# Kernel optimization log

Measured on AMD Instinct MI355X. Metric: run time of the kernel, lower is better.

## Reference

```python
import jax, jax.numpy as jnp
import numpy as np

N_NODES = 100000
N_EDGES = 1200000
NODE_IN = 64
EDGE_IN = 32
HIDDEN = 64


def _glorot(key, shape):
    fan_in, fan_out = shape[0], shape[1]
    s = jnp.sqrt(2.0 / (fan_in + fan_out))
    return jax.random.normal(key, shape, dtype=jnp.float32) * s


def setup_inputs() -> dict:
    key = jax.random.key(0)
    ks = jax.random.split(key, 16)
    inp = {
        "x": jax.random.normal(ks[0], (N_NODES, NODE_IN), dtype=jnp.float32),
        "edge_index": jax.random.randint(ks[1], (2, N_EDGES), 0, N_NODES, dtype=jnp.int64),
        "edge_attr": jax.random.normal(ks[2], (N_EDGES, EDGE_IN), dtype=jnp.float32),
        # SAGE layer 0 (in=NODE_IN -> HIDDEN): lin_l (neighbors, has bias), lin_r (root)
        "w_l0": _glorot(ks[3], (NODE_IN, HIDDEN)),
        "w_r0": _glorot(ks[4], (NODE_IN, HIDDEN)),
        "b0": jnp.zeros((HIDDEN,), jnp.float32),
        "ln_g0": jnp.ones((HIDDEN,), jnp.float32),
        "ln_b0": jnp.zeros((HIDDEN,), jnp.float32),
        # SAGE layer 1 (HIDDEN -> HIDDEN)
        "w_l1": _glorot(ks[5], (HIDDEN, HIDDEN)),
        "w_r1": _glorot(ks[6], (HIDDEN, HIDDEN)),
        "b1": jnp.zeros((HIDDEN,), jnp.float32),
        "ln_g1": jnp.ones((HIDDEN,), jnp.float32),
        "ln_b1": jnp.zeros((HIDDEN,), jnp.float32),
        # Edge classifier MLP: in_dim = 3*HIDDEN + EDGE_IN = 224
        "cw1": _glorot(ks[7], (3 * HIDDEN + EDGE_IN, HIDDEN)),
        "cb1": jnp.zeros((HIDDEN,), jnp.float32),
        "cw2": _glorot(ks[8], (HIDDEN, HIDDEN // 2)),
        "cb2": jnp.zeros((HIDDEN // 2,), jnp.float32),
        "cw3": _glorot(ks[9], (HIDDEN // 2, 1)),
        "cb3": jnp.zeros((1,), jnp.float32),
    }
    return inp


def _sage_conv(x, src, dst, w_l, w_r, b):
    # mean-aggregate source features at destination nodes (PyG SAGEConv, aggr='mean')
    n = x.shape[0]
    msg = x[src]  # [E, F] gather
    agg = jax.ops.segment_sum(msg, dst, num_segments=n)
    cnt = jax.ops.segment_sum(jnp.ones((src.shape[0], 1), x.dtype), dst, num_segments=n)
    mean = agg / jnp.maximum(cnt, 1.0)
    return mean @ w_l + x @ w_r + b


def _layer_norm(x, g, b, eps=1e-5):
    mu = jnp.mean(x, axis=-1, keepdims=True)
    var = jnp.var(x, axis=-1, keepdims=True)
    return (x - mu) * jax.lax.rsqrt(var + eps) * g + b


def reference(x, edge_index, edge_attr,
              w_l0, w_r0, b0, ln_g0, ln_b0,
              w_l1, w_r1, b1, ln_g1, ln_b1,
              cw1, cb1, cw2, cb2, cw3, cb3):
    src, dst = edge_index[0], edge_index[1]
    # Encoder (eval mode: dropout is identity)
    h = jax.nn.relu(_layer_norm(_sage_conv(x, src, dst, w_l0, w_r0, b0), ln_g0, ln_b0))
    z = jax.nn.relu(_layer_norm(_sage_conv(h, src, dst, w_l1, w_r1, b1), ln_g1, ln_b1))
    # Edge classifier: gather-concat-MLP
    z_src = z[src]
    z_dst = z[dst]
    edge_repr = jnp.concatenate([z_src, z_dst, z_src * z_dst, edge_attr], axis=-1)
    h1 = jax.nn.relu(edge_repr @ cw1 + cb1)
    h2 = jax.nn.relu(h1 @ cw2 + cb2)
    logits = (h2 @ cw3 + cb3).squeeze(-1)  # [E]
    return logits
```

## Files before the change

kernel.cpp:

```cpp
#include <hip/hip_runtime.h>
#include <hip/hip_bf16.h>

#define N_NODES 100000
#define N_EDGES 1200000

typedef __attribute__((ext_vector_type(8))) short bfrag;
typedef __attribute__((ext_vector_type(4))) float ffrag;

union FragU { uint4 v; uint32_t u[4]; bfrag f; };

__device__ __forceinline__ ushort bfbits(float a) {
  union { __hip_bfloat16 h; ushort u; } c; c.h = __float2bfloat16(a); return c.u;
}
__device__ __forceinline__ uint32_t pkbf(float a, float b) {
  union { __hip_bfloat162 h; uint32_t u; } c;
  c.h = __float22bfloat162_rn(float2{a, b}); return c.u;
}
__device__ __forceinline__ uint32_t mul2bf(uint32_t a, uint32_t b) {
  union { uint32_t u; __hip_bfloat162 h; } x, y, r;
  x.u = a; y.u = b; r.h = __hmul2(x.h, y.h); return r.u;
}
__device__ __forceinline__ float bflo(uint32_t u) { return __int_as_float(u << 16); }
__device__ __forceinline__ float bfhi(uint32_t u) { return __int_as_float(u & 0xffff0000u); }


__global__ void cvt_k(const float* __restrict__ x, ushort* __restrict__ xb, int n2) {
  int i = blockIdx.x * blockDim.x + threadIdx.x;
  if (i < n2) {
    float2 v = ((const float2*)x)[i];
    ((uint32_t*)xb)[i] = pkbf(v.x, v.y);
  }
}


__global__ void hist_k(const int* __restrict__ ei, int* __restrict__ deg, int E) {
  int e = blockIdx.x * blockDim.x + threadIdx.x;
  if (e < E) atomicAdd(&deg[ei[E + e]], 1);
}

__global__ __launch_bounds__(1024) void scan1_k(const int* __restrict__ deg,
                                                int* __restrict__ off,
                                                int* __restrict__ bsum, int n) {
  __shared__ int wpart[16];
  __shared__ int wpre[16];
  int tid = threadIdx.x, lane = tid & 63, wid = tid >> 6;
  int i = blockIdx.x * 1024 + tid;
  int v = (i < n) ? deg[i] : 0;
  int x = v;
  #pragma unroll
  for (int o = 1; o < 64; o <<= 1) {
    int y = __shfl_up(x, o);
    if (lane >= o) x += y;
  }
  if (lane == 63) wpart[wid] = x;
  __syncthreads();
  if (tid == 0) {
    int run = 0;
    #pragma unroll
    for (int w = 0; w < 16; w++) { int t = wpart[w]; wpre[w] = run; run += t; }
    bsum[blockIdx.x] = run;
  }
  __syncthreads();
  if (i < n) off[i] = x - v + wpre[wid];
}

__global__ void scan2_k(const int* __restrict__ bsum, int* __restrict__ bpre,
                        int* __restrict__ off, int nb, int n) {
  if (threadIdx.x == 0) {
    int run = 0;
    for (int b = 0; b < nb; b++) { int t = bsum[b]; bpre[b] = run; run += t; }
    off[n] = run;
  }
}

__global__ __launch_bounds__(1024) void scan3_k(int* __restrict__ off, int* __restrict__ pos,
                                                const int* __restrict__ bpre, int n) {
  int i = blockIdx.x * 1024 + threadIdx.x;
  if (i < n) {
    int o = off[i] + bpre[blockIdx.x];
    off[i] = o;
    pos[i] = o;
  }
}

__global__ void fill_k(const int* __restrict__ ei, int* __restrict__ pos,
                       int* __restrict__ csr, int E) {
  int e = blockIdx.x * blockDim.x + threadIdx.x;
  if (e < E) {
    int d = ei[E + e];
    int p = atomicAdd(&pos[d], 1);
    csr[p] = ei[e];
  }
}


__global__ __launch_bounds__(256) void agg_k(
    const ushort* __restrict__ Xb, const int* __restrict__ off, const int* __restrict__ csr,
    ushort* __restrict__ aggout, int n) {
  int lane = threadIdx.x & 63;
  int quad = lane >> 4, f8 = lane & 15;
  int wave = blockIdx.x * 4 + (threadIdx.x >> 6);
  int nw = gridDim.x * 4;
  int nquads = (n + 3) >> 2;
  const uint2* X2 = (const uint2*)Xb;
  for (int p = wave; p < nquads; p += nw) {
    int i = p * 4 + quad;
    int ic = i < n ? i : n - 1;
    int s0 = off[ic], s1 = off[ic + 1];
    float a0 = 0.f, a1 = 0.f, a2 = 0.f, a3 = 0.f;
    for (int j = s0; j < s1; j += 8) {
      int id[8]; uint2 us[8];
      #pragma unroll
      for (int u = 0; u < 8; u++) {
        int jj = j + u;
        id[u] = csr[jj < s1 ? jj : s1 - 1];
      }
      #pragma unroll
      for (int u = 0; u < 8; u++) us[u] = X2[(size_t)id[u] * 16 + f8];
      #pragma unroll
      for (int u = 0; u < 8; u++) {
        if (j + u < s1) {
          a0 += bflo(us[u].x); a1 += bfhi(us[u].x);
          a2 += bflo(us[u].y); a3 += bfhi(us[u].y);
        }
      }
    }
    if (i < n) {
      float rdeg = 1.f / fmaxf((float)(s1 - s0), 1.f);
      uint2 w;
      w.x = pkbf(a0 * rdeg, a1 * rdeg);
      w.y = pkbf(a2 * rdeg, a3 * rdeg);
      ((uint2*)aggout)[(size_t)i * 16 + f8] = w;
    }
  }
}


__global__ __launch_bounds__(256) void node_k(
    const ushort* __restrict__ agg, const ushort* __restrict__ selfb,
    const float* __restrict__ wl, const float* __restrict__ wr,
    const float* __restrict__ bias, const float* __restrict__ g, const float* __restrict__ lb,
    ushort* __restrict__ outb, int n) {
  __shared__ ushort wt[64 * 128];
  const int tid = threadIdx.x;
  for (int i = tid; i < 8192; i += 256) {
    int k = i >> 6, nn = i & 63;
    float v = (k < 64) ? wl[k * 64 + nn] : wr[(k - 64) * 64 + nn];
    wt[nn * 128 + (((k >> 3) ^ (nn & 7)) * 8) + (k & 7)] = bfbits(v);
  }
  __syncthreads();
  const int lane = tid & 63, wid = tid >> 6;
  const int ln = lane & 15, q = lane >> 4;
  float bias_n[4], g_n[4], lb_n[4];
  #pragma unroll
  for (int nt = 0; nt < 4; nt++) {
    bias_n[nt] = bias[nt * 16 + ln];
    g_n[nt] = g[nt * 16 + ln];
    lb_n[nt] = lb[nt * 16 + ln];
  }
  const int ntiles = (n + 15) >> 4;
  for (int t = blockIdx.x * 4 + wid; t < ntiles; t += gridDim.x * 4) {
    int node = t * 16 + ln;
    int nc = node < n ? node : n - 1;
    FragU afr[4];
    #pragma unroll
    for (int kk = 0; kk < 2; kk++) {
      afr[kk].v     = ((const uint4*)agg)[(size_t)nc * 8 + kk * 4 + q];
      afr[2 + kk].v = ((const uint4*)selfb)[(size_t)nc * 8 + kk * 4 + q];
    }
    ffrag acc[4];
    #pragma unroll
    for (int nt = 0; nt < 4; nt++) acc[nt] = ffrag{0.f, 0.f, 0.f, 0.f};
    #pragma unroll
    for (int kk = 0; kk < 4; kk++) {
      bfrag a = afr[kk].f;
      #pragma unroll
      for (int nt = 0; nt < 4; nt++) {
        int nn = nt * 16 + ln;
        int b = kk * 4 + q;
        const bfrag* bp = (const bfrag*)&wt[nn * 128 + ((b ^ (nn & 7)) * 8)];
        acc[nt] = __builtin_amdgcn_mfma_f32_16x16x32_bf16(a, *bp, acc[nt], 0, 0, 0);
      }
    }
    #pragma unroll
    for (int r = 0; r < 4; r++) {
      int m = t * 16 + q * 4 + r;
      float o[4];
      #pragma unroll
      for (int nt = 0; nt < 4; nt++) o[nt] = acc[nt][r] + bias_n[nt];
      float s = (o[0] + o[1]) + (o[2] + o[3]);
      #pragma unroll
      for (int mm = 1; mm < 16; mm <<= 1) s += __shfl_xor(s, mm);
      float mu = s * (1.f / 64.f);
      float v2 = 0.f;
      #pragma unroll
      for (int nt = 0; nt < 4; nt++) { float d2 = o[nt] - mu; v2 += d2 * d2; }
      #pragma unroll
      for (int mm = 1; mm < 16; mm <<= 1) v2 += __shfl_xor(v2, mm);
      float rs = rsqrtf(v2 * (1.f / 64.f) + 1e-5f);
      if (m < n) {
        #pragma unroll
        for (int nt = 0; nt < 4; nt++) {
          float y = fmaxf((o[nt] - mu) * rs * g_n[nt] + lb_n[nt], 0.f);
          outb[(size_t)m * 64 + nt * 16 + ln] = bfbits(y);
        }
      }
    }
  }
}


__global__ __launch_bounds__(256, 2) void edge_mfma_k(
    const int* __restrict__ ei, const float* __restrict__ ea,
    const ushort* __restrict__ zb,
    const float* __restrict__ cw1, const float* __restrict__ cb1,
    const float* __restrict__ cw2, const float* __restrict__ cb2,
    const float* __restrict__ cw3, const float* __restrict__ cb3,
    float* __restrict__ out, int E) {
  __shared__ ushort h1b[4][16 * 64];
  const int tid = threadIdx.x;
  const int lane = tid & 63, wid = tid >> 6;
  const int ln = lane & 15, q = lane >> 4;

  FragU w1f[7][4];
  #pragma unroll
  for (int kk = 0; kk < 7; kk++) {
    #pragma unroll
    for (int tt = 0; tt < 4; tt++) {
      #pragma unroll
      for (int p = 0; p < 4; p++) {
        int k = (kk * 4 + q) * 8 + p * 2;
        int n = tt * 16 + ln;
        w1f[kk][tt].u[p] = pkbf(cw1[k * 64 + n], cw1[(k + 1) * 64 + n]);
      }
    }
  }
  FragU w2f[2][2];
  #pragma unroll
  for (int t2 = 0; t2 < 2; t2++) {
    #pragma unroll
    for (int kk = 0; kk < 2; kk++) {
      #pragma unroll
      for (int p = 0; p < 4; p++) {
        int k = kk * 32 + q * 8 + p * 2;
        int n = t2 * 16 + ln;
        w2f[t2][kk].u[p] = pkbf(cw2[k * 32 + n], cw2[(k + 1) * 32 + n]);
      }
    }
  }

  float cb1v[4];
  #pragma unroll
  for (int t = 0; t < 4; t++) cb1v[t] = cb1[t * 16 + ln];
  float cb2a = cb2[ln], cb2b = cb2[16 + ln];
  float w3a = cw3[ln], w3b = cw3[16 + ln];
  float cb3v = cb3[0];

  ushort* hb = h1b[wid];
  const int ntiles = E >> 4;
  for (int t = blockIdx.x * 4 + wid; t < ntiles; t += gridDim.x * 4) {
    int e = t * 16 + ln;
    int s = ei[e], d = ei[E + e];

    FragU afr[7];
    #pragma unroll
    for (int kk = 0; kk < 2; kk++) {
      afr[kk].v     = ((const uint4*)zb)[(size_t)s * 8 + kk * 4 + q];
      afr[2 + kk].v = ((const uint4*)zb)[(size_t)d * 8 + kk * 4 + q];
    }
    {
      float4 lo = ((const float4*)ea)[(size_t)e * 8 + q * 2];
      float4 hi = ((const float4*)ea)[(size_t)e * 8 + q * 2 + 1];
      afr[6].u[0] = pkbf(lo.x, lo.y); afr[6].u[1] = pkbf(lo.z, lo.w);
      afr[6].u[2] = pkbf(hi.x, hi.y); afr[6].u[3] = pkbf(hi.z, hi.w);
    }
    #pragma unroll
    for (int kk = 0; kk < 2; kk++) {
      #pragma unroll
      for (int p = 0; p < 4; p++)
        afr[4 + kk].u[p] = mul2bf(afr[kk].u[p], afr[2 + kk].u[p]);
    }

    ffrag acc1[4];
    #pragma unroll
    for (int tt = 0; tt < 4; tt++) acc1[tt] = ffrag{0.f, 0.f, 0.f, 0.f};
    #pragma unroll
    for (int kk = 0; kk < 7; kk++) {
      bfrag a = afr[kk].f;
      #pragma unroll
      for (int tt = 0; tt < 4; tt++)
        acc1[tt] = __builtin_amdgcn_mfma_f32_16x16x32_bf16(a, w1f[kk][tt].f, acc1[tt], 0, 0, 0);
    }

    #pragma unroll
    for (int tt = 0; tt < 4; tt++) {
      #pragma unroll
      for (int r = 0; r < 4; r++) {
        int m = q * 4 + r;
        int col = tt * 16 + ln;
        float v = fmaxf(acc1[tt][r] + cb1v[tt], 0.f);
        hb[m * 64 + (((col >> 3) ^ (m & 7)) * 8) + (col & 7)] = bfbits(v);
      }
    }

    ffrag acc2[2];
    acc2[0] = ffrag{0.f, 0.f, 0.f, 0.f};
    acc2[1] = ffrag{0.f, 0.f, 0.f, 0.f};
    #pragma unroll
    for (int kk = 0; kk < 2; kk++) {
      int b = kk * 4 + q;
      const bfrag* ap = (const bfrag*)&hb[ln * 64 + ((b ^ (ln & 7)) * 8)];
      bfrag a2 = *ap;
      acc2[0] = __builtin_amdgcn_mfma_f32_16x16x32_bf16(a2, w2f[0][kk].f, acc2[0], 0, 0, 0);
      acc2[1] = __builtin_amdgcn_mfma_f32_16x16x32_bf16(a2, w2f[1][kk].f, acc2[1], 0, 0, 0);
    }

    float p0, p1, p2, p3;
    {
      p0 = fmaxf(acc2[0][0] + cb2a, 0.f) * w3a + fmaxf(acc2[1][0] + cb2b, 0.f) * w3b;
      p1 = fmaxf(acc2[0][1] + cb2a, 0.f) * w3a + fmaxf(acc2[1][1] + cb2b, 0.f) * w3b;
      p2 = fmaxf(acc2[0][2] + cb2a, 0.f) * w3a + fmaxf(acc2[1][2] + cb2b, 0.f) * w3b;
      p3 = fmaxf(acc2[0][3] + cb2a, 0.f) * w3a + fmaxf(acc2[1][3] + cb2b, 0.f) * w3b;
    }
    #pragma unroll
    for (int o = 1; o < 16; o <<= 1) {
      p0 += __shfl_xor(p0, o);
      p1 += __shfl_xor(p1, o);
      p2 += __shfl_xor(p2, o);
      p3 += __shfl_xor(p3, o);
    }
    float keep = (ln == 0) ? p0 : (ln == 1) ? p1 : (ln == 2) ? p2 : p3;
    if (ln < 4) out[t * 16 + q * 4 + ln] = keep + cb3v;
  }
}


extern "C" void kernel_launch(void* const* d_in, const int* in_sizes, int n_in,
                              void* d_out, int out_size, void* d_ws, size_t ws_size,
                              hipStream_t stream) {
  const float* x   = (const float*)d_in[0];
  const int*   ei  = (const int*)d_in[1];
  const float* ea  = (const float*)d_in[2];
  const float* wl0 = (const float*)d_in[3];
  const float* wr0 = (const float*)d_in[4];
  const float* b0  = (const float*)d_in[5];
  const float* g0  = (const float*)d_in[6];
  const float* lb0 = (const float*)d_in[7];
  const float* wl1 = (const float*)d_in[8];
  const float* wr1 = (const float*)d_in[9];
  const float* b1  = (const float*)d_in[10];
  const float* g1  = (const float*)d_in[11];
  const float* lb1 = (const float*)d_in[12];
  const float* cw1 = (const float*)d_in[13];
  const float* cb1 = (const float*)d_in[14];
  const float* cw2 = (const float*)d_in[15];
  const float* cb2 = (const float*)d_in[16];
  const float* cw3 = (const float*)d_in[17];
  const float* cb3 = (const float*)d_in[18];
  float* out = (float*)d_out;
  const int N = N_NODES, E = N_EDGES;
  const int NB = (N + 1023) / 1024;

  uintptr_t pp = (uintptr_t)d_ws;
  auto alloc = [&](size_t bytes) {
    uintptr_t r = (pp + 255) & ~(uintptr_t)255; pp = r + bytes; return (void*)r;
  };
  int* deg  = (int*)alloc((size_t)N * 4);
  int* off  = (int*)alloc((size_t)(N + 1) * 4);
  int* pos  = (int*)alloc((size_t)N * 4);
  int* csr  = (int*)alloc((size_t)E * 4);
  int* bsum = (int*)alloc((size_t)NB * 4);
  int* bpre = (int*)alloc((size_t)NB * 4);
  ushort* xb  = (ushort*)alloc((size_t)N * 64 * 2);
  ushort* agg = (ushort*)alloc((size_t)N * 64 * 2);
  ushort* hb  = (ushort*)alloc((size_t)N * 64 * 2);
  ushort* zb  = (ushort*)alloc((size_t)N * 64 * 2);

  hipMemsetAsync(deg, 0, (size_t)N * 4, stream);
  cvt_k<<<(N * 32 + 255) / 256, 256, 0, stream>>>(x, xb, N * 32);
  hist_k<<<(E + 255) / 256, 256, 0, stream>>>(ei, deg, E);
  scan1_k<<<NB, 1024, 0, stream>>>(deg, off, bsum, N);
  scan2_k<<<1, 64, 0, stream>>>(bsum, bpre, off, NB, N);
  scan3_k<<<NB, 1024, 0, stream>>>(off, pos, bpre, N);
  fill_k<<<(E + 255) / 256, 256, 0, stream>>>(ei, pos, csr, E);
  agg_k<<<2048, 256, 0, stream>>>(xb, off, csr, agg, N);
  node_k<<<512, 256, 0, stream>>>(agg, xb, wl0, wr0, b0, g0, lb0, hb, N);
  agg_k<<<2048, 256, 0, stream>>>(hb, off, csr, agg, N);
  node_k<<<512, 256, 0, stream>>>(agg, hb, wl1, wr1, b1, g1, lb1, zb, N);
  edge_mfma_k<<<512, 256, 0, stream>>>(ei, ea, zb, cw1, cb1, cw2, cb2, cw3, cb3, out, E);
}
```

Baseline: 561.2 us.

## Prefetch next edge tile, stage classifier weights in LDS, atomic-free CSR fill

The edge classifier now keeps the first-layer weights in swizzled LDS instead of 112 VGPRs per lane. This frees registers so the launch-bounds occupancy hint can be dropped and the grid doubled. It also software-pipelines the gather of the next tile's node embeddings and edge attributes behind the current tile's MFMA work. The CSR build records each edge's rank from the histogram atomic and fills without a second atomic pass, using nontemporal stores. Costs are extra LDS reads per MFMA, a per-block weight staging step, and an extra E-sized rank buffer.

```diff
diff --git a/kernel.cpp b/kernel.cpp
--- a/kernel.cpp
+++ b/kernel.cpp
@@ -33,9 +33,10 @@
 }
 
 
-__global__ void hist_k(const int* __restrict__ ei, int* __restrict__ deg, int E) {
+__global__ void hist_k(const int* __restrict__ ei, int* __restrict__ deg,
+                       int* __restrict__ rank, int E) {
   int e = blockIdx.x * blockDim.x + threadIdx.x;
-  if (e < E) atomicAdd(&deg[ei[E + e]], 1);
+  if (e < E) rank[e] = atomicAdd(&deg[ei[E + e]], 1);
 }
 
 __global__ __launch_bounds__(1024) void scan1_k(const int* __restrict__ deg,
@@ -73,23 +74,19 @@
   }
 }
 
-__global__ __launch_bounds__(1024) void scan3_k(int* __restrict__ off, int* __restrict__ pos,
+__global__ __launch_bounds__(1024) void scan3_k(int* __restrict__ off,
                                                 const int* __restrict__ bpre, int n) {
   int i = blockIdx.x * 1024 + threadIdx.x;
-  if (i < n) {
-    int o = off[i] + bpre[blockIdx.x];
-    off[i] = o;
-    pos[i] = o;
-  }
-}
-
-__global__ void fill_k(const int* __restrict__ ei, int* __restrict__ pos,
-                       int* __restrict__ csr, int E) {
+  if (i < n) off[i] += bpre[blockIdx.x];
+}
+
+__global__ void fill_k(const int* __restrict__ ei, const int* __restrict__ off,
+                       const int* __restrict__ rank, int* __restrict__ csr, int E) {
   int e = blockIdx.x * blockDim.x + threadIdx.x;
   if (e < E) {
     int d = ei[E + e];
-    int p = atomicAdd(&pos[d], 1);
-    csr[p] = ei[e];
+    int p = off[d] + rank[e];
+    __builtin_nontemporal_store(ei[e], &csr[p]);
   }
 }
 
@@ -210,44 +207,26 @@
 }
 
 
-__global__ __launch_bounds__(256, 2) void edge_mfma_k(
+__global__ __launch_bounds__(256) void edge_mfma_k(
     const int* __restrict__ ei, const float* __restrict__ ea,
     const ushort* __restrict__ zb,
     const float* __restrict__ cw1, const float* __restrict__ cb1,
     const float* __restrict__ cw2, const float* __restrict__ cb2,
     const float* __restrict__ cw3, const float* __restrict__ cb3,
     float* __restrict__ out, int E) {
+  __shared__ ushort wt1[64 * 256];
   __shared__ ushort h1b[4][16 * 64];
   const int tid = threadIdx.x;
+
+  for (int i = tid; i < 224 * 64; i += 256) {
+    int k = i >> 6, n = i & 63;
+    int blk = k >> 3;
+    wt1[n * 256 + ((blk ^ (n & 7)) * 8) + (k & 7)] = bfbits(cw1[i]);
+  }
+  __syncthreads();
+
   const int lane = tid & 63, wid = tid >> 6;
   const int ln = lane & 15, q = lane >> 4;
-
-  FragU w1f[7][4];
-  #pragma unroll
-  for (int kk = 0; kk < 7; kk++) {
-    #pragma unroll
-    for (int tt = 0; tt < 4; tt++) {
-      #pragma unroll
-      for (int p = 0; p < 4; p++) {
-        int k = (kk * 4 + q) * 8 + p * 2;
-        int n = tt * 16 + ln;
-        w1f[kk][tt].u[p] = pkbf(cw1[k * 64 + n], cw1[(k + 1) * 64 + n]);
-      }
-    }
-  }
-  FragU w2f[2][2];
-  #pragma unroll
-  for (int t2 = 0; t2 < 2; t2++) {
-    #pragma unroll
-    for (int kk = 0; kk < 2; kk++) {
-      #pragma unroll
-      for (int p = 0; p < 4; p++) {
-        int k = kk * 32 + q * 8 + p * 2;
-        int n = t2 * 16 + ln;
-        w2f[t2][kk].u[p] = pkbf(cw2[k * 32 + n], cw2[(k + 1) * 32 + n]);
-      }
-    }
-  }
 
   float cb1v[4];
   #pragma unroll
@@ -256,30 +235,61 @@
   float w3a = cw3[ln], w3b = cw3[16 + ln];
   float cb3v = cb3[0];
 
+  FragU w2f[2][2];
+  #pragma unroll
+  for (int t2 = 0; t2 < 2; t2++) {
+    #pragma unroll
+    for (int kk = 0; kk < 2; kk++) {
+      #pragma unroll
+      for (int p = 0; p < 4; p++) {
+        int k = kk * 32 + q * 8 + p * 2;
+        int n = t2 * 16 + ln;
+        w2f[t2][kk].u[p] = pkbf(cw2[k * 32 + n], cw2[(k + 1) * 32 + n]);
+      }
+    }
+  }
+
   ushort* hb = h1b[wid];
   const int ntiles = E >> 4;
-  for (int t = blockIdx.x * 4 + wid; t < ntiles; t += gridDim.x * 4) {
+  const int stride = gridDim.x * 4;
+  int t = blockIdx.x * 4 + wid;
+
+  FragU curz[4]; float4 ceal, ceah;
+  if (t < ntiles) {
     int e = t * 16 + ln;
     int s = ei[e], d = ei[E + e];
+    curz[0].v = ((const uint4*)zb)[(size_t)s * 8 + q];
+    curz[1].v = ((const uint4*)zb)[(size_t)s * 8 + 4 + q];
+    curz[2].v = ((const uint4*)zb)[(size_t)d * 8 + q];
+    curz[3].v = ((const uint4*)zb)[(size_t)d * 8 + 4 + q];
+    ceal = ((const float4*)ea)[(size_t)e * 8 + q * 2];
+    ceah = ((const float4*)ea)[(size_t)e * 8 + q * 2 + 1];
+  }
+
+  for (; t < ntiles; t += stride) {
+    int tn = t + stride;
+    FragU nz[4]; float4 neal, neah;
+    if (tn < ntiles) {
+      int e2 = tn * 16 + ln;
+      int s2 = ei[e2], d2 = ei[E + e2];
+      nz[0].v = ((const uint4*)zb)[(size_t)s2 * 8 + q];
+      nz[1].v = ((const uint4*)zb)[(size_t)s2 * 8 + 4 + q];
+      nz[2].v = ((const uint4*)zb)[(size_t)d2 * 8 + q];
+      nz[3].v = ((const uint4*)zb)[(size_t)d2 * 8 + 4 + q];
+      neal = ((const float4*)ea)[(size_t)e2 * 8 + q * 2];
+      neah = ((const float4*)ea)[(size_t)e2 * 8 + q * 2 + 1];
+    }
 
     FragU afr[7];
+    afr[0] = curz[0]; afr[1] = curz[1]; afr[2] = curz[2]; afr[3] = curz[3];
     #pragma unroll
     for (int kk = 0; kk < 2; kk++) {
-      afr[kk].v     = ((const uint4*)zb)[(size_t)s * 8 + kk * 4 + q];
-      afr[2 + kk].v = ((const uint4*)zb)[(size_t)d * 8 + kk * 4 + q];
-    }
-    {
-      float4 lo = ((const float4*)ea)[(size_t)e * 8 + q * 2];
-      float4 hi = ((const float4*)ea)[(size_t)e * 8 + q * 2 + 1];
-      afr[6].u[0] = pkbf(lo.x, lo.y); afr[6].u[1] = pkbf(lo.z, lo.w);
-      afr[6].u[2] = pkbf(hi.x, hi.y); afr[6].u[3] = pkbf(hi.z, hi.w);
-    }
-    #pragma unroll
-    for (int kk = 0; kk < 2; kk++) {
       #pragma unroll
       for (int p = 0; p < 4; p++)
-        afr[4 + kk].u[p] = mul2bf(afr[kk].u[p], afr[2 + kk].u[p]);
-    }
+        afr[4 + kk].u[p] = mul2bf(curz[kk].u[p], curz[2 + kk].u[p]);
+    }
+    afr[6].u[0] = pkbf(ceal.x, ceal.y); afr[6].u[1] = pkbf(ceal.z, ceal.w);
+    afr[6].u[2] = pkbf(ceah.x, ceah.y); afr[6].u[3] = pkbf(ceah.z, ceah.w);
 
     ffrag acc1[4];
     #pragma unroll
@@ -288,8 +298,12 @@
     for (int kk = 0; kk < 7; kk++) {
       bfrag a = afr[kk].f;
       #pragma unroll
-      for (int tt = 0; tt < 4; tt++)
-        acc1[tt] = __builtin_amdgcn_mfma_f32_16x16x32_bf16(a, w1f[kk][tt].f, acc1[tt], 0, 0, 0);
+      for (int tt = 0; tt < 4; tt++) {
+        int n = tt * 16 + ln;
+        int b = kk * 4 + q;
+        const bfrag* bp = (const bfrag*)&wt1[n * 256 + ((b ^ (n & 7)) * 8)];
+        acc1[tt] = __builtin_amdgcn_mfma_f32_16x16x32_bf16(a, *bp, acc1[tt], 0, 0, 0);
+      }
     }
 
     #pragma unroll
@@ -331,6 +345,9 @@
     }
     float keep = (ln == 0) ? p0 : (ln == 1) ? p1 : (ln == 2) ? p2 : p3;
     if (ln < 4) out[t * 16 + q * 4 + ln] = keep + cb3v;
+
+    curz[0] = nz[0]; curz[1] = nz[1]; curz[2] = nz[2]; curz[3] = nz[3];
+    ceal = neal; ceah = neah;
   }
 }
 
@@ -367,7 +384,7 @@
   };
   int* deg  = (int*)alloc((size_t)N * 4);
   int* off  = (int*)alloc((size_t)(N + 1) * 4);
-  int* pos  = (int*)alloc((size_t)N * 4);
+  int* rank = (int*)alloc((size_t)E * 4);
   int* csr  = (int*)alloc((size_t)E * 4);
   int* bsum = (int*)alloc((size_t)NB * 4);
   int* bpre = (int*)alloc((size_t)NB * 4);
@@ -378,14 +395,14 @@
 
   hipMemsetAsync(deg, 0, (size_t)N * 4, stream);
   cvt_k<<<(N * 32 + 255) / 256, 256, 0, stream>>>(x, xb, N * 32);
-  hist_k<<<(E + 255) / 256, 256, 0, stream>>>(ei, deg, E);
+  hist_k<<<(E + 255) / 256, 256, 0, stream>>>(ei, deg, rank, E);
   scan1_k<<<NB, 1024, 0, stream>>>(deg, off, bsum, N);
   scan2_k<<<1, 64, 0, stream>>>(bsum, bpre, off, NB, N);
-  scan3_k<<<NB, 1024, 0, stream>>>(off, pos, bpre, N);
-  fill_k<<<(E + 255) / 256, 256, 0, stream>>>(ei, pos, csr, E);
+  scan3_k<<<NB, 1024, 0, stream>>>(off, bpre, N);
+  fill_k<<<(E + 255) / 256, 256, 0, stream>>>(ei, off, rank, csr, E);
   agg_k<<<2048, 256, 0, stream>>>(xb, off, csr, agg, N);
   node_k<<<512, 256, 0, stream>>>(agg, xb, wl0, wr0, b0, g0, lb0, hb, N);
   agg_k<<<2048, 256, 0, stream>>>(hb, off, csr, agg, N);
   node_k<<<512, 256, 0, stream>>>(agg, hb, wl1, wr1, b1, g1, lb1, zb, N);
-  edge_mfma_k<<<512, 256, 0, stream>>>(ei, ea, zb, cw1, cb1, cw2, cb2, cw3, cb3, out, E);
-}
+  edge_mfma_k<<<1024, 256, 0, stream>>>(ei, ea, zb, cw1, cb1, cw2, cb2, cw3, cb3, out, E);
+}
```

Measured after the change: 515.1 us. 8.2% less time.
